# Performance work log

Measured on AMD Instinct MI355X. Metric: run time of the kernel, lower is better.

## Reference

```python
import jax, jax.numpy as jnp
import numpy as np

DIM, NH, WS, SR, CTS = 256, 8, 8, 4, 2
HD = DIM // NH
SCALE = HD ** -0.5

def _linear(x, w, b=None):
    y = x @ w.T
    return y + b if b is not None else y

def _ln(x, g, b, eps=1e-5):
    m = jnp.mean(x, -1, keepdims=True)
    v = jnp.mean((x - m) ** 2, -1, keepdims=True)
    return (x - m) / jnp.sqrt(v + eps) * g + b

def _mlp(x, w1, b1, w2, b2):
    return _linear(jax.nn.gelu(_linear(x, w1, b1), approximate=False), w2, b2)

def _pos_emb_rank3(seq_len, w1, b1, w2):
    # PosEmbMLPSwinv1D with rank=3: coords on cube_root(seq) grid, normalized
    s = int(round(seq_len ** (1.0 / 3.0)))
    c = (jnp.arange(s, dtype=jnp.float32) - s // 2) / (s // 2)
    grid = jnp.stack(jnp.meshgrid(c, c, c, indexing='ij'))      # (3,s,s,s)
    tbl = grid.reshape(3, -1).T                                 # (s^3,3)
    return _linear(jax.nn.relu(_linear(tbl, w1, b1)), w2)[None]  # (1,s^3,dim)

def _rel_bias_3d(ws, w1, b1, w2, n_global):
    # PosEmbMLPSwinv3D: CPB-MLP bias over 3D relative coords, 16*sigmoid, zero-pad for carrier tokens
    r = jnp.arange(-(ws - 1), ws, dtype=jnp.float32)
    tbl = jnp.stack(jnp.meshgrid(r, r, r, indexing='ij'), axis=-1) / (ws - 1)
    tbl = tbl * 8.0
    tbl = jnp.sign(tbl) * jnp.log2(jnp.abs(tbl) + 1.0) / np.log2(8.0)
    table = _linear(jax.nn.relu(_linear(tbl.reshape(-1, 3), w1, b1)), w2)  # ((2ws-1)^3, NH)
    coords = jnp.stack(jnp.meshgrid(jnp.arange(ws), jnp.arange(ws), jnp.arange(ws), indexing='ij'))
    cf = coords.reshape(3, -1)
    rel = (cf[:, :, None] - cf[:, None, :]).transpose(1, 2, 0) + (ws - 1)  # (P,P,3)
    idx = rel[..., 0] * (2 * ws - 1) ** 2 + rel[..., 1] * (2 * ws - 1) + rel[..., 2]
    P = ws ** 3
    bias = table[idx.reshape(-1)].reshape(P, P, NH).transpose(2, 0, 1)
    bias = 16.0 * jax.nn.sigmoid(bias)
    return jnp.pad(bias, ((0, 0), (n_global, 0), (n_global, 0)))[None]  # (1,NH,P+g,P+g)

def _win_attn(x, qkv_w, qkv_b, proj_w, proj_b, bias):
    B, N, C = x.shape
    qkv = _linear(x, qkv_w, qkv_b).reshape(B, N, 3, NH, HD).transpose(2, 0, 3, 1, 4)
    q, k, v = qkv[0], qkv[1], qkv[2]
    attn = jax.nn.softmax(jnp.einsum('bhnd,bhmd->bhnm', q, k) * SCALE + bias, axis=-1)
    out = jnp.einsum('bhnm,bhmd->bhnd', attn, v).transpose(0, 2, 1, 3).reshape(B, N, C)
    return _linear(out, proj_w, proj_b)

def _ct_dewindow(ct, W, H, D, ws):
    bs, _, N = ct.shape
    c = ct.reshape(bs, W // ws, H // ws, D // ws, ws, ws, ws, N)
    c = c.transpose(0, 7, 1, 3, 5, 2, 4, 6).reshape(bs, N, W * H * D)
    return c.transpose(0, 2, 1)

def _ct_window(ct, W, H, D, ws):
    bs, _, N = ct.shape
    c = ct.reshape(bs, H // ws, ws, W // ws, ws, D // ws, ws, N)
    return c.transpose(0, 1, 3, 5, 2, 4, 6, 7)

def setup_inputs() -> dict:
    key = jax.random.key(0)
    ks = jax.random.split(key, 48)
    B0 = 1
    nw = SR ** 3
    def w(k, *s):
        return jax.random.normal(k, s, jnp.float32) * 0.02
    def b(k, *s):
        return jax.random.normal(k, s, jnp.float32) * 0.01
    d4 = 4 * DIM
    return {
        'x': jax.random.normal(ks[0], (B0 * nw, WS ** 3, DIM), jnp.float32),
        'ct': jax.random.normal(ks[1], (B0, (CTS * SR) ** 3, DIM), jnp.float32),
        'pe_w1': w(ks[2], 512, 3), 'pe_b1': b(ks[3], 512), 'pe_w2': w(ks[4], DIM, 512),
        'hpe_w1': w(ks[5], 512, 3), 'hpe_b1': b(ks[6], 512), 'hpe_w2': w(ks[7], DIM, 512),
        'hat_n1_g': jnp.ones((DIM,), jnp.float32), 'hat_n1_b': jnp.zeros((DIM,), jnp.float32),
        'hat_qkv_w': w(ks[8], 3 * DIM, DIM), 'hat_qkv_b': b(ks[9], 3 * DIM),
        'hat_proj_w': w(ks[10], DIM, DIM), 'hat_proj_b': b(ks[11], DIM),
        'hat_cpb_w1': w(ks[12], 512, 3), 'hat_cpb_b1': b(ks[13], 512), 'hat_cpb_w2': w(ks[14], NH, 512),
        'hat_n2_g': jnp.ones((DIM,), jnp.float32), 'hat_n2_b': jnp.zeros((DIM,), jnp.float32),
        'hat_fc1_w': w(ks[15], d4, DIM), 'hat_fc1_b': b(ks[16], d4),
        'hat_fc2_w': w(ks[17], DIM, d4), 'hat_fc2_b': b(ks[18], DIM),
        'n1_g': jnp.ones((DIM,), jnp.float32), 'n1_b': jnp.zeros((DIM,), jnp.float32),
        'qkv_w': w(ks[19], 3 * DIM, DIM), 'qkv_b': b(ks[20], 3 * DIM),
        'proj_w': w(ks[21], DIM, DIM), 'proj_b': b(ks[22], DIM),
        'cpb_w1': w(ks[23], 512, 3), 'cpb_b1': b(ks[24], 512), 'cpb_w2': w(ks[25], NH, 512),
        'n2_g': jnp.ones((DIM,), jnp.float32), 'n2_b': jnp.zeros((DIM,), jnp.float32),
        'fc1_w': w(ks[26], d4, DIM), 'fc1_b': b(ks[27], d4),
        'fc2_w': w(ks[28], DIM, d4), 'fc2_b': b(ks[29], DIM),
    }

def reference(x, ct, pe_w1, pe_b1, pe_w2, hpe_w1, hpe_b1, hpe_w2,
              hat_n1_g, hat_n1_b, hat_qkv_w, hat_qkv_b, hat_proj_w, hat_proj_b,
              hat_cpb_w1, hat_cpb_b1, hat_cpb_w2, hat_n2_g, hat_n2_b,
              hat_fc1_w, hat_fc1_b, hat_fc2_w, hat_fc2_b,
              n1_g, n1_b, qkv_w, qkv_b, proj_w, proj_b,
              cpb_w1, cpb_b1, cpb_w2, n2_g, n2_b, fc1_w, fc1_b, fc2_w, fc2_b):
    Bg, Ng, Hg = ct.shape
    G = CTS * SR  # carrier-token global cube side
    x = x + _pos_emb_rank3(x.shape[1], pe_w1, pe_b1, pe_w2)
    # carrier-token global attention (hierarchical path)
    ct = _ct_dewindow(ct, G, G, G, CTS)
    ct = ct + _pos_emb_rank3(ct.shape[1], hpe_w1, hpe_b1, hpe_w2)
    hat_bias = _rel_bias_3d(G, hat_cpb_w1, hat_cpb_b1, hat_cpb_w2, 0)
    ct = ct + _win_attn(_ln(ct, hat_n1_g, hat_n1_b), hat_qkv_w, hat_qkv_b, hat_proj_w, hat_proj_b, hat_bias)
    ct = ct + _mlp(_ln(ct, hat_n2_g, hat_n2_b), hat_fc1_w, hat_fc1_b, hat_fc2_w, hat_fc2_b)
    ct_w = _ct_window(ct, G, G, G, CTS).reshape(x.shape[0], -1, Hg)
    # windowed attention over [carrier tokens ; window tokens]
    x = jnp.concatenate([ct_w, x], axis=1)
    bias = _rel_bias_3d(WS, cpb_w1, cpb_b1, cpb_w2, CTS ** 3)
    x = x + _win_attn(_ln(x, n1_g, n1_b), qkv_w, qkv_b, proj_w, proj_b, bias)
    x = x + _mlp(_ln(x, n2_g, n2_b), fc1_w, fc1_b, fc2_w, fc2_b)
    split = x.shape[1] - WS ** 3
    ctr, x = x[:, :split], x[:, split:]
    return x, ctr.reshape(Bg, Ng, Hg)
```

## Files before the change

kernel.cpp:

```cpp
#include <hip/hip_runtime.h>
#include <hip/hip_bf16.h>
#include <math.h>

typedef __hip_bfloat16 bf16;

#define SCALE_QK 0.17677669529663687f

__device__ __forceinline__ float b2f(bf16 v){ return __bfloat162float(v); }
__device__ __forceinline__ bf16  f2b(float v){ return __float2bfloat16(v); }
__device__ __forceinline__ short bfs(float x){ bf16 b = f2b(x); short s; __builtin_memcpy(&s, &b, 2); return s; }

struct __align__(16) bf16x8 { bf16 v[8]; };

typedef __attribute__((ext_vector_type(8))) short sh8;
typedef __attribute__((ext_vector_type(4))) short sh4;
typedef __attribute__((ext_vector_type(4))) float f4;

#if defined(__has_builtin)
#if __has_builtin(__builtin_amdgcn_mfma_f32_16x16x16bf16_1k)
#define HAS_MFMA16 1
#else
#define HAS_MFMA16 0
#endif
#else
#define HAS_MFMA16 0
#endif

__global__ __launch_bounds__(256) void wcvt10_k(const float* s0, const float* s1, const float* s2, const float* s3,
                                                const float* s4, const float* s5, const float* s6, const float* s7,
                                                const float* s8, const float* s9,
                                                bf16* d0, bf16* d1, bf16* d2, bf16* d3, bf16* d4,
                                                bf16* d5, bf16* d6, bf16* d7, bf16* d8, bf16* d9) {
    const int sizes[10] = {196608, 65536, 262144, 262144, 196608, 65536, 262144, 262144, 131072, 131072};
    int which = blockIdx.y;
    const float* s; bf16* d;
    switch (which) {
        case 0: s = s0; d = d0; break;  case 1: s = s1; d = d1; break;
        case 2: s = s2; d = d2; break;  case 3: s = s3; d = d3; break;
        case 4: s = s4; d = d4; break;  case 5: s = s5; d = d5; break;
        case 6: s = s6; d = d6; break;  case 7: s = s7; d = d7; break;
        case 8: s = s8; d = d8; break;  default: s = s9; d = d9; break;
    }
    int i = blockIdx.x * 256 + threadIdx.x;
    if (i < sizes[which]) d[i] = f2b(s[i]);
}

__global__ __launch_bounds__(256) void hidbuild_k(const float* __restrict__ w1a, const float* __restrict__ b1a,
                                                  const float* __restrict__ w1b, const float* __restrict__ b1b,
                                                  bf16* __restrict__ hidA, bf16* __restrict__ hidB) {
    const float* w1 = blockIdx.y ? w1b : w1a;
    const float* b1 = blockIdx.y ? b1b : b1a;
    bf16* hid       = blockIdx.y ? hidB : hidA;
    int t = blockIdx.x, tid = threadIdx.x;
    int i = t >> 6, j = (t >> 3) & 7, k = t & 7;
    float c0 = (i - 4) * 0.25f, c1 = (j - 4) * 0.25f, c2 = (k - 4) * 0.25f;
    #pragma unroll
    for (int rep = 0; rep < 2; rep++) {
        int jj = tid + rep * 256;
        float h = c0 * w1[jj*3+0] + c1 * w1[jj*3+1] + c2 * w1[jj*3+2] + b1[jj];
        hid[(size_t)t * 512 + jj] = f2b(fmaxf(h, 0.f));
    }
}

__device__ __forceinline__ float cpb_coord(int idx) {
    float v = (idx - 7) * (8.0f / 7.0f);
    return copysignf(log2f(fabsf(v) + 1.0f) * (1.0f / 3.0f), v);
}
__global__ __launch_bounds__(512) void cpbtab_k(const float* __restrict__ w1a, const float* __restrict__ b1a,
                                                const float* __restrict__ w2a, float* __restrict__ taba,
                                                const float* __restrict__ w1b, const float* __restrict__ b1b,
                                                const float* __restrict__ w2b, float* __restrict__ tabb) {
    const float* w1 = blockIdx.y ? w1b : w1a;
    const float* b1 = blockIdx.y ? b1b : b1a;
    const float* w2 = blockIdx.y ? w2b : w2a;
    float* tab      = blockIdx.y ? tabb : taba;
    int t = blockIdx.x, tid = threadIdx.x;
    __shared__ float hid[512];
    int i = t / 225, r = t - i * 225, j = r / 15, k = r - j * 15;
    float x0 = cpb_coord(i), x1 = cpb_coord(j), x2 = cpb_coord(k);
    float h = x0 * w1[tid*3+0] + x1 * w1[tid*3+1] + x2 * w1[tid*3+2] + b1[tid];
    hid[tid] = fmaxf(h, 0.f);
    __syncthreads();
    int h8 = tid >> 6, lane = tid & 63;
    float p = 0.f;
    for (int jj = lane; jj < 512; jj += 64) p += hid[jj] * w2[h8*512 + jj];
    for (int off = 32; off; off >>= 1) p += __shfl_down(p, off);
    if (lane == 0) tab[t * 8 + h8] = p;
}

__global__ __launch_bounds__(256) void biasbuild_k(const float* __restrict__ taba, float* __restrict__ biasQa,
                                                   const float* __restrict__ tabb, float* __restrict__ biasQb) {
    const float* tab = blockIdx.y ? tabb : taba;
    float* biasQ     = blockIdx.y ? biasQb : biasQa;
    int idx = blockIdx.x * 256 + threadIdx.x;
    int h = idx >> 18, rem = idx & 262143;
    int q = rem >> 9, k = rem & 511;
    int qx = q >> 6, qy = (q >> 3) & 7, qz = q & 7;
    int kx = k >> 6, ky = (k >> 3) & 7, kz = k & 7;
    int tidx = ((qx - kx + 7) * 15 + (qy - ky + 7)) * 15 + (qz - kz + 7);
    float v = tab[tidx * 8 + h];
    biasQ[idx] = 16.f / (1.f + __expf(-v));
}

__global__ __launch_bounds__(256) void ct0build_k(const float* __restrict__ ct_in,
                                                  const float* __restrict__ hpe,
                                                  float* __restrict__ ct0) {
    int u = blockIdx.x, c = threadIdx.x;
    int a = u >> 7, cc = (u >> 5) & 3, e = (u >> 4) & 1, b = (u >> 2) & 3, d = (u >> 1) & 1, f = u & 1;
    int t = a * 128 + b * 32 + cc * 8 + d * 4 + e * 2 + f;
    ct0[(size_t)u * 256 + c] = ct_in[(size_t)t * 256 + c] + hpe[(size_t)u * 256 + c];
}

__global__ __launch_bounds__(256) void ln_k(const float* __restrict__ in,
                                            const float* __restrict__ g,
                                            const float* __restrict__ b,
                                            bf16* __restrict__ out) {
    int row = blockIdx.x, c = threadIdx.x;
    float x = in[(size_t)row * 256 + c];
    float s = x, s2 = x * x;
    for (int off = 32; off; off >>= 1) { s += __shfl_down(s, off); s2 += __shfl_down(s2, off); }
    __shared__ float red[8];
    int wid = c >> 6, lane = c & 63;
    if (lane == 0) { red[wid] = s; red[wid + 4] = s2; }
    __syncthreads();
    if (c == 0) { red[0] = red[0] + red[1] + red[2] + red[3]; red[4] = red[4] + red[5] + red[6] + red[7]; }
    __syncthreads();
    float mean = red[0] * (1.f / 256.f);
    float var  = fmaxf(red[4] * (1.f / 256.f) - mean * mean, 0.f);
    float rstd = rsqrtf(var + 1e-5f);
    out[(size_t)row * 256 + c] = f2b((x - mean) * rstd * g[c] + b[c]);
}

template <int MODE>
__global__ __launch_bounds__(256) void gemm_k(const bf16* __restrict__ A,
                                              const bf16* __restrict__ W,
                                              const float* __restrict__ bias,
                                              int M, int N, int K,
                                              float* __restrict__ res,
                                              bf16* __restrict__ outb) {
    __shared__ short As[128 * 40];
    __shared__ short Ws[128 * 40];
    int m0 = blockIdx.y * 128, n0 = blockIdx.x * 128;
    int tid = threadIdx.x;
    int lane = tid & 63, wave = tid >> 6;
    int quad = lane >> 4, m16 = lane & 15;
    int wm = (wave & 1) * 64, wn = (wave >> 1) * 64;
    int arow = tid >> 2, acol = (tid & 3) * 8;

    f4 acc[4][4];
    #pragma unroll
    for (int i = 0; i < 4; i++)
        #pragma unroll
        for (int j = 0; j < 4; j++) acc[i][j] = (f4){0.f, 0.f, 0.f, 0.f};

    for (int k0 = 0; k0 < K; k0 += 32) {
        sh8 a0 = *reinterpret_cast<const sh8*>(A + (size_t)(m0 + arow) * K + k0 + acol);
        sh8 a1 = *reinterpret_cast<const sh8*>(A + (size_t)(m0 + arow + 64) * K + k0 + acol);
        sh8 w0 = *reinterpret_cast<const sh8*>(W + (size_t)(n0 + arow) * K + k0 + acol);
        sh8 w1 = *reinterpret_cast<const sh8*>(W + (size_t)(n0 + arow + 64) * K + k0 + acol);
        __syncthreads();
        *reinterpret_cast<sh8*>(&As[arow * 40 + acol])        = a0;
        *reinterpret_cast<sh8*>(&As[(arow + 64) * 40 + acol]) = a1;
        *reinterpret_cast<sh8*>(&Ws[arow * 40 + acol])        = w0;
        *reinterpret_cast<sh8*>(&Ws[(arow + 64) * 40 + acol]) = w1;
        __syncthreads();
        sh8 af[4], bf[4];
        #pragma unroll
        for (int mi = 0; mi < 4; mi++)
            af[mi] = *reinterpret_cast<const sh8*>(&As[(wm + mi * 16 + m16) * 40 + quad * 8]);
        #pragma unroll
        for (int ni = 0; ni < 4; ni++)
            bf[ni] = *reinterpret_cast<const sh8*>(&Ws[(wn + ni * 16 + m16) * 40 + quad * 8]);
        #pragma unroll
        for (int mi = 0; mi < 4; mi++)
            #pragma unroll
            for (int ni = 0; ni < 4; ni++)
                acc[mi][ni] = __builtin_amdgcn_mfma_f32_16x16x32_bf16(af[mi], bf[ni], acc[mi][ni], 0, 0, 0);
    }
    (void)M;

    #pragma unroll
    for (int mi = 0; mi < 4; mi++) {
        #pragma unroll
        for (int r = 0; r < 4; r++) {
            int gm = m0 + wm + mi * 16 + quad * 4 + r;
            #pragma unroll
            for (int ni = 0; ni < 4; ni++) {
                int gn = n0 + wn + ni * 16 + m16;
                float v = acc[mi][ni][r];
                if constexpr (MODE != 3) v += bias[gn];
                if constexpr (MODE == 2)      res[(size_t)gm * N + gn] += v;
                else if constexpr (MODE == 3) res[(size_t)gm * N + gn] = v;
                else if constexpr (MODE == 1) outb[(size_t)gm * N + gn] = f2b(0.5f * v * (1.0f + erff(v * 0.70710678118654752f)));
                else                          outb[(size_t)gm * N + gn] = f2b(v);
            }
        }
    }
}

#define VSTR 548
#define FIXM 24.0f
__global__ __launch_bounds__(512) void flash_k(const bf16* __restrict__ qkv,
                                               const float* __restrict__ biasQ,
                                               bf16* __restrict__ out,
                                               int N, int glob) {
    int wh = blockIdx.x, w = wh >> 3, h = wh & 7;
    int qs = blockIdx.y, QS = gridDim.y;
    int tid = threadIdx.x;
    int lane = tid & 63, wave = tid >> 6;
    int quad = lane >> 4, qcol = lane & 15;
    const int NT32 = (N + 31) & ~31;

    __shared__ bf16  Vt[32 * VSTR];
    __shared__ float Osm[8 * 528];
#if !HAS_MFMA16
    __shared__ float Ps[8][16 * 17];
#endif

    for (int i = tid; i < NT32 * 4; i += 512) {
        int tok = i >> 2, seg = i & 3;
        if (tok < N) {
            const bf16* vp = qkv + ((size_t)(w * N + tok)) * 768 + 512 + h * 32 + seg * 8;
            bf16x8 vv = *reinterpret_cast<const bf16x8*>(vp);
            #pragma unroll
            for (int e = 0; e < 8; e++) Vt[(seg * 8 + e) * VSTR + tok] = vv.v[e];
        } else {
            bf16 z = f2b(0.f);
            #pragma unroll
            for (int e = 0; e < 8; e++) Vt[(seg * 8 + e) * VSTR + tok] = z;
        }
    }
    __syncthreads();

    const bf16* qbase = qkv + ((size_t)w * N) * 768 + h * 32;
    const bf16* kbase = qbase + 256;
    int nqt = (N + 15) >> 4, nkt = NT32 >> 5;

    for (int qt = wave + 8 * qs; qt < nqt; qt += 8 * QS) {
        int q_idx = qt * 16 + qcol;
        int q_rd  = (q_idx < N) ? q_idx : (N - 1);
        sh8 qfrag = *reinterpret_cast<const sh8*>(qbase + (size_t)q_rd * 768 + quad * 8);
        f4 O0 = {0.f, 0.f, 0.f, 0.f}, O1 = {0.f, 0.f, 0.f, 0.f};
        float l = 0.f;
        bool qb = (q_idx >= glob) && (q_idx < N);
        const float* brow = biasQ + (((size_t)h << 9) + (size_t)(qb ? (q_idx - glob) : 0)) * 512 - glob;

        for (int kt = 0; kt < nkt; kt++) {
            int bt = kt * 32;
            int k0 = bt + qcol, k1 = bt + 16 + qcol;
            sh8 kf0 = *reinterpret_cast<const sh8*>(kbase + (size_t)((k0 < N) ? k0 : (N - 1)) * 768 + quad * 8);
            sh8 kf1 = *reinterpret_cast<const sh8*>(kbase + (size_t)((k1 < N) ? k1 : (N - 1)) * 768 + quad * 8);
            f4 z = {0.f, 0.f, 0.f, 0.f};
            f4 s0 = __builtin_amdgcn_mfma_f32_16x16x32_bf16(kf0, qfrag, z, 0, 0, 0);
            f4 s1 = __builtin_amdgcn_mfma_f32_16x16x32_bf16(kf1, qfrag, z, 0, 0, 0);

            int tg0 = bt + quad * 4, tg1 = bt + 16 + quad * 4;
            float p[8];
            {
                f4 bb = {0.f, 0.f, 0.f, 0.f};
                if (qb && tg0 >= glob) bb = *reinterpret_cast<const f4*>(brow + tg0);
                bool valid = tg0 < N;
                #pragma unroll
                for (int r = 0; r < 4; r++)
                    p[r] = valid ? __expf(fmaf(s0[r], SCALE_QK, bb[r]) - FIXM) : 0.f;
            }
            {
                f4 bb = {0.f, 0.f, 0.f, 0.f};
                if (qb && tg1 >= glob && tg1 < N) bb = *reinterpret_cast<const f4*>(brow + tg1);
                bool valid = tg1 < N;
                #pragma unroll
                for (int r = 0; r < 4; r++)
                    p[4 + r] = valid ? __expf(fmaf(s1[r], SCALE_QK, bb[r]) - FIXM) : 0.f;
            }
            #pragma unroll
            for (int r = 0; r < 8; r++) l += p[r];

#if HAS_MFMA16
            sh4 pf0, pf1;
            #pragma unroll
            for (int r = 0; r < 4; r++) { pf0[r] = bfs(p[r]); pf1[r] = bfs(p[4 + r]); }
            sh4 v00 = *reinterpret_cast<const sh4*>(&Vt[qcol * VSTR + bt + quad * 4]);
            sh4 v10 = *reinterpret_cast<const sh4*>(&Vt[qcol * VSTR + bt + 16 + quad * 4]);
            sh4 v01 = *reinterpret_cast<const sh4*>(&Vt[(qcol + 16) * VSTR + bt + quad * 4]);
            sh4 v11 = *reinterpret_cast<const sh4*>(&Vt[(qcol + 16) * VSTR + bt + 16 + quad * 4]);
            O0 = __builtin_amdgcn_mfma_f32_16x16x16bf16_1k(v00, pf0, O0, 0, 0, 0);
            O0 = __builtin_amdgcn_mfma_f32_16x16x16bf16_1k(v10, pf1, O0, 0, 0, 0);
            O1 = __builtin_amdgcn_mfma_f32_16x16x16bf16_1k(v01, pf0, O1, 0, 0, 0);
            O1 = __builtin_amdgcn_mfma_f32_16x16x16bf16_1k(v11, pf1, O1, 0, 0, 0);
#else
            for (int half = 0; half < 2; half++) {
                #pragma unroll
                for (int r = 0; r < 4; r++) Ps[wave][(quad * 4 + r) * 17 + qcol] = p[half * 4 + r];
                __builtin_amdgcn_wave_barrier();
                sh8 pbig, va, vb;
                #pragma unroll
                for (int j = 0; j < 8; j++) {
                    int tl = quad * 8 + j;
                    float pv = (quad < 2) ? Ps[wave][tl * 17 + qcol] : 0.f;
                    pbig[j] = bfs(pv);
                    bf16 a0 = (quad < 2) ? Vt[qcol * VSTR + bt + half * 16 + tl] : f2b(0.f);
                    bf16 a1 = (quad < 2) ? Vt[(qcol + 16) * VSTR + bt + half * 16 + tl] : f2b(0.f);
                    short t0, t1;
                    __builtin_memcpy(&t0, &a0, 2); __builtin_memcpy(&t1, &a1, 2);
                    va[j] = t0; vb[j] = t1;
                }
                O0 = __builtin_amdgcn_mfma_f32_16x16x32_bf16(va, pbig, O0, 0, 0, 0);
                O1 = __builtin_amdgcn_mfma_f32_16x16x32_bf16(vb, pbig, O1, 0, 0, 0);
                __builtin_amdgcn_wave_barrier();
            }
#endif
        }

        l += __shfl_xor(l, 16);
        l += __shfl_xor(l, 32);
        float rl = 1.f / l;
        #pragma unroll
        for (int r = 0; r < 4; r++) {
            Osm[wave * 528 + qcol * 33 + quad * 4 + r]      = O0[r] * rl;
            Osm[wave * 528 + qcol * 33 + 16 + quad * 4 + r] = O1[r] * rl;
        }
        __builtin_amdgcn_wave_barrier();
        int row = lane >> 2, dseg = (lane & 3) * 8;
        int q_out = qt * 16 + row;
        if (q_out < N) {
            bf16x8 ov;
            #pragma unroll
            for (int e = 0; e < 8; e++) ov.v[e] = f2b(Osm[wave * 528 + row * 33 + dseg + e]);
            *reinterpret_cast<bf16x8*>(out + ((size_t)(w * N + q_out)) * 256 + h * 32 + dseg) = ov;
        }
        __builtin_amdgcn_wave_barrier();
    }
}

__global__ __launch_bounds__(256) void xcatbuild_k(const float* __restrict__ x_in,
                                                   const float* __restrict__ pe,
                                                   const float* __restrict__ ct2,
                                                   float* __restrict__ xcat) {
    int row = blockIdx.x, w = row / 520, p = row - w * 520, c = threadIdx.x;
    float v;
    if (p < 8) {
        int P = w >> 4, Q = (w >> 2) & 3, R = w & 3;
        int S = p >> 2, T = (p >> 1) & 1, U = p & 1;
        int t = P * 128 + S * 64 + Q * 16 + T * 8 + R * 2 + U;
        v = ct2[(size_t)t * 256 + c];
    } else {
        int t = p - 8;
        v = x_in[((size_t)w * 512 + t) * 256 + c] + pe[(size_t)t * 256 + c];
    }
    xcat[(size_t)row * 256 + c] = v;
}

__global__ __launch_bounds__(256) void outbuild_k(const float* __restrict__ xcat,
                                                  float* __restrict__ out) {
    int row = blockIdx.x, w = row / 520, p = row - w * 520, c = threadIdx.x;
    float v = xcat[(size_t)row * 256 + c];
    if (p >= 8) out[((size_t)(w * 512) + (p - 8)) * 256 + c] = v;
    else        out[(size_t)8388608 + ((size_t)(w * 8) + p) * 256 + c] = v;
}

extern "C" void kernel_launch(void* const* d_in, const int* in_sizes, int n_in,
                              void* d_out, int out_size, void* d_ws, size_t ws_size,
                              hipStream_t stream) {
    const float* x          = (const float*)d_in[0];
    const float* ct         = (const float*)d_in[1];
    const float* pe_w1      = (const float*)d_in[2];
    const float* pe_b1      = (const float*)d_in[3];
    const float* pe_w2      = (const float*)d_in[4];
    const float* hpe_w1     = (const float*)d_in[5];
    const float* hpe_b1     = (const float*)d_in[6];
    const float* hpe_w2     = (const float*)d_in[7];
    const float* hat_n1_g   = (const float*)d_in[8];
    const float* hat_n1_b   = (const float*)d_in[9];
    const float* hat_qkv_w  = (const float*)d_in[10];
    const float* hat_qkv_b  = (const float*)d_in[11];
    const float* hat_proj_w = (const float*)d_in[12];
    const float* hat_proj_b = (const float*)d_in[13];
    const float* hat_cpb_w1 = (const float*)d_in[14];
    const float* hat_cpb_b1 = (const float*)d_in[15];
    const float* hat_cpb_w2 = (const float*)d_in[16];
    const float* hat_n2_g   = (const float*)d_in[17];
    const float* hat_n2_b   = (const float*)d_in[18];
    const float* hat_fc1_w  = (const float*)d_in[19];
    const float* hat_fc1_b  = (const float*)d_in[20];
    const float* hat_fc2_w  = (const float*)d_in[21];
    const float* hat_fc2_b  = (const float*)d_in[22];
    const float* n1_g       = (const float*)d_in[23];
    const float* n1_b       = (const float*)d_in[24];
    const float* qkv_w      = (const float*)d_in[25];
    const float* qkv_b      = (const float*)d_in[26];
    const float* proj_w     = (const float*)d_in[27];
    const float* proj_b     = (const float*)d_in[28];
    const float* cpb_w1     = (const float*)d_in[29];
    const float* cpb_b1     = (const float*)d_in[30];
    const float* cpb_w2     = (const float*)d_in[31];
    const float* n2_g       = (const float*)d_in[32];
    const float* n2_b       = (const float*)d_in[33];
    const float* fc1_w      = (const float*)d_in[34];
    const float* fc1_b      = (const float*)d_in[35];
    const float* fc2_w      = (const float*)d_in[36];
    const float* fc2_b      = (const float*)d_in[37];
    (void)in_sizes; (void)n_in; (void)out_size;

    char* base = (char*)d_ws;
    size_t off = 0;
    auto alloc = [&](size_t bytes) -> void* {
        void* p = base + off;
        off += (bytes + 255) & ~(size_t)255;
        return p;
    };
    float* pe        = (float*)alloc(512 * 256 * 4);
    float* hpe       = (float*)alloc(512 * 256 * 4);
    float* tab_hat   = (float*)alloc(3375 * 8 * 4);
    float* tab2      = (float*)alloc(3375 * 8 * 4);
    float* biasQ2    = (float*)alloc((size_t)8 * 512 * 512 * 4);
    float* ct0       = (float*)alloc(512 * 256 * 4);
    bf16* wb_hqkv  = (bf16*)alloc(768 * 256 * 2);
    bf16* wb_hproj = (bf16*)alloc(256 * 256 * 2);
    bf16* wb_hfc1  = (bf16*)alloc(1024 * 256 * 2);
    bf16* wb_hfc2  = (bf16*)alloc(256 * 1024 * 2);
    bf16* wb_qkv   = (bf16*)alloc(768 * 256 * 2);
    bf16* wb_proj  = (bf16*)alloc(256 * 256 * 2);
    bf16* wb_fc1   = (bf16*)alloc(1024 * 256 * 2);
    bf16* wb_fc2   = (bf16*)alloc(256 * 1024 * 2);
    bf16* wb_pew2  = (bf16*)alloc(256 * 512 * 2);
    bf16* wb_hpew2 = (bf16*)alloc(256 * 512 * 2);
    size_t zstart = off;
    bf16*  hidA      = (bf16*)alloc(512 * 512 * 2);
    bf16*  hidB      = (bf16*)alloc(512 * 512 * 2);
    off = zstart;
    float* biasQ_hat = (float*)alloc((size_t)8 * 512 * 512 * 4);
    bf16*  hct_ln    = (bf16*)alloc(512 * 256 * 2);
    bf16*  hqkv      = (bf16*)alloc(512 * 768 * 2);
    bf16*  hat_attn  = (bf16*)alloc(512 * 256 * 2);
    bf16*  hat_hid   = (bf16*)alloc(512 * 1024 * 2);
    off = zstart;
    float* xcat      = (float*)alloc((size_t)64 * 520 * 256 * 4);
    const int S     = (ws_size >= (size_t)150 * 1024 * 1024) ? 1 : 4;
    const int rows  = 33280 / S;
    const int wins  = 64 / S;
    bf16*  xln_b     = (bf16*)alloc((size_t)rows * 256 * 2);
    char*  region_qa = (char*)alloc((size_t)rows * 1024 * 2);
    bf16*  qkv_b_    = (bf16*)region_qa;
    bf16*  attn_b    = (bf16*)(region_qa + (size_t)rows * 768 * 2);
    bf16*  hidden    = (bf16*)region_qa;

    wcvt10_k<<<dim3(1024, 10), 256, 0, stream>>>(hat_qkv_w, hat_proj_w, hat_fc1_w, hat_fc2_w,
                                                 qkv_w, proj_w, fc1_w, fc2_w, pe_w2, hpe_w2,
                                                 wb_hqkv, wb_hproj, wb_hfc1, wb_hfc2,
                                                 wb_qkv, wb_proj, wb_fc1, wb_fc2, wb_pew2, wb_hpew2);

    hidbuild_k<<<dim3(512, 2), 256, 0, stream>>>(pe_w1, pe_b1, hpe_w1, hpe_b1, hidA, hidB);
    gemm_k<3><<<dim3(2, 4), 256, 0, stream>>>(hidA, wb_pew2,  nullptr, 512, 256, 512, pe,  nullptr);
    gemm_k<3><<<dim3(2, 4), 256, 0, stream>>>(hidB, wb_hpew2, nullptr, 512, 256, 512, hpe, nullptr);

    cpbtab_k<<<dim3(3375, 2), 512, 0, stream>>>(hat_cpb_w1, hat_cpb_b1, hat_cpb_w2, tab_hat,
                                                cpb_w1, cpb_b1, cpb_w2, tab2);
    biasbuild_k<<<dim3(8192, 2), 256, 0, stream>>>(tab_hat, biasQ_hat, tab2, biasQ2);

    ct0build_k<<<512, 256, 0, stream>>>(ct, hpe, ct0);
    ln_k<<<512, 256, 0, stream>>>(ct0, hat_n1_g, hat_n1_b, hct_ln);
    gemm_k<0><<<dim3(6, 4), 256, 0, stream>>>(hct_ln, wb_hqkv, hat_qkv_b, 512, 768, 256, nullptr, hqkv);
    flash_k<<<dim3(8, 4), 512, 0, stream>>>(hqkv, biasQ_hat, hat_attn, 512, 0);
    gemm_k<2><<<dim3(2, 4), 256, 0, stream>>>(hat_attn, wb_hproj, hat_proj_b, 512, 256, 256, ct0, nullptr);
    ln_k<<<512, 256, 0, stream>>>(ct0, hat_n2_g, hat_n2_b, hct_ln);
    gemm_k<1><<<dim3(8, 4), 256, 0, stream>>>(hct_ln, wb_hfc1, hat_fc1_b, 512, 1024, 256, nullptr, hat_hid);
    gemm_k<2><<<dim3(2, 4), 256, 0, stream>>>(hat_hid, wb_hfc2, hat_fc2_b, 512, 256, 1024, ct0, nullptr);

    xcatbuild_k<<<33280, 256, 0, stream>>>(x, pe, ct0, xcat);

    for (int s = 0; s < S; s++) {
        float* xc = xcat + (size_t)s * rows * 256;
        ln_k<<<rows, 256, 0, stream>>>(xc, n1_g, n1_b, xln_b);
        gemm_k<0><<<dim3(6, rows / 128), 256, 0, stream>>>(xln_b, wb_qkv, qkv_b, rows, 768, 256, nullptr, qkv_b_);
        flash_k<<<dim3(wins * 8, 5), 512, 0, stream>>>(qkv_b_, biasQ2, attn_b, 520, 8);
        gemm_k<2><<<dim3(2, rows / 128), 256, 0, stream>>>(attn_b, wb_proj, proj_b, rows, 256, 256, xc, nullptr);
    }
    for (int s = 0; s < S; s++) {
        float* xc = xcat + (size_t)s * rows * 256;
        ln_k<<<rows, 256, 0, stream>>>(xc, n2_g, n2_b, xln_b);
        gemm_k<1><<<dim3(8, rows / 128), 256, 0, stream>>>(xln_b, wb_fc1, fc1_b, rows, 1024, 256, nullptr, hidden);
        gemm_k<2><<<dim3(2, rows / 128), 256, 0, stream>>>(hidden, wb_fc2, fc2_b, rows, 256, 1024, xc, nullptr);
    }

    outbuild_k<<<33280, 256, 0, stream>>>(xcat, (float*)d_out);
}
```

Baseline: 648.0 us.

## Process two query tiles per wave in flash attention and prefetch K fragments

```diff
diff --git a/kernel.cpp b/kernel.cpp
--- a/kernel.cpp
+++ b/kernel.cpp
@@ -235,98 +235,154 @@
     const bf16* qbase = qkv + ((size_t)w * N) * 768 + h * 32;
     const bf16* kbase = qbase + 256;
     int nqt = (N + 15) >> 4, nkt = NT32 >> 5;
-
-    for (int qt = wave + 8 * qs; qt < nqt; qt += 8 * QS) {
-        int q_idx = qt * 16 + qcol;
-        int q_rd  = (q_idx < N) ? q_idx : (N - 1);
-        sh8 qfrag = *reinterpret_cast<const sh8*>(qbase + (size_t)q_rd * 768 + quad * 8);
-        f4 O0 = {0.f, 0.f, 0.f, 0.f}, O1 = {0.f, 0.f, 0.f, 0.f};
-        float l = 0.f;
-        bool qb = (q_idx >= glob) && (q_idx < N);
-        const float* brow = biasQ + (((size_t)h << 9) + (size_t)(qb ? (q_idx - glob) : 0)) * 512 - glob;
+    int npt = (nqt + 1) >> 1;
+
+    for (int pp = wave + 8 * qs; pp < npt; pp += 8 * QS) {
+        int qA = pp * 32 + qcol;
+        int qB = qA + 16;
+        int qrA = (qA < N) ? qA : (N - 1);
+        int qrB = (qB < N) ? qB : (N - 1);
+        sh8 qfA = *reinterpret_cast<const sh8*>(qbase + (size_t)qrA * 768 + quad * 8);
+        sh8 qfB = *reinterpret_cast<const sh8*>(qbase + (size_t)qrB * 768 + quad * 8);
+        f4 O0A = {0.f,0.f,0.f,0.f}, O1A = {0.f,0.f,0.f,0.f};
+        f4 O0B = {0.f,0.f,0.f,0.f}, O1B = {0.f,0.f,0.f,0.f};
+        float lA = 0.f, lB = 0.f;
+        bool vA = (qA >= glob) && (qA < N);
+        bool vB = (qB >= glob) && (qB < N);
+        const float* browA = biasQ + (((size_t)h << 9) + (size_t)(vA ? (qA - glob) : 0)) * 512 - glob;
+        const float* browB = biasQ + (((size_t)h << 9) + (size_t)(vB ? (qB - glob) : 0)) * 512 - glob;
+
+        sh8 kf0, kf1;
+        {
+            int k0 = qcol, k1 = 16 + qcol;
+            kf0 = *reinterpret_cast<const sh8*>(kbase + (size_t)((k0 < N) ? k0 : (N - 1)) * 768 + quad * 8);
+            kf1 = *reinterpret_cast<const sh8*>(kbase + (size_t)((k1 < N) ? k1 : (N - 1)) * 768 + quad * 8);
+        }
 
         for (int kt = 0; kt < nkt; kt++) {
             int bt = kt * 32;
-            int k0 = bt + qcol, k1 = bt + 16 + qcol;
-            sh8 kf0 = *reinterpret_cast<const sh8*>(kbase + (size_t)((k0 < N) ? k0 : (N - 1)) * 768 + quad * 8);
-            sh8 kf1 = *reinterpret_cast<const sh8*>(kbase + (size_t)((k1 < N) ? k1 : (N - 1)) * 768 + quad * 8);
+            sh8 c0 = kf0, c1 = kf1;
+            if (kt + 1 < nkt) {
+                int n0 = bt + 32 + qcol, n1 = bt + 48 + qcol;
+                kf0 = *reinterpret_cast<const sh8*>(kbase + (size_t)((n0 < N) ? n0 : (N - 1)) * 768 + quad * 8);
+                kf1 = *reinterpret_cast<const sh8*>(kbase + (size_t)((n1 < N) ? n1 : (N - 1)) * 768 + quad * 8);
+            }
             f4 z = {0.f, 0.f, 0.f, 0.f};
-            f4 s0 = __builtin_amdgcn_mfma_f32_16x16x32_bf16(kf0, qfrag, z, 0, 0, 0);
-            f4 s1 = __builtin_amdgcn_mfma_f32_16x16x32_bf16(kf1, qfrag, z, 0, 0, 0);
+            f4 s0A = __builtin_amdgcn_mfma_f32_16x16x32_bf16(c0, qfA, z, 0, 0, 0);
+            f4 s1A = __builtin_amdgcn_mfma_f32_16x16x32_bf16(c1, qfA, z, 0, 0, 0);
+            f4 s0B = __builtin_amdgcn_mfma_f32_16x16x32_bf16(c0, qfB, z, 0, 0, 0);
+            f4 s1B = __builtin_amdgcn_mfma_f32_16x16x32_bf16(c1, qfB, z, 0, 0, 0);
 
             int tg0 = bt + quad * 4, tg1 = bt + 16 + quad * 4;
-            float p[8];
-            {
-                f4 bb = {0.f, 0.f, 0.f, 0.f};
-                if (qb && tg0 >= glob) bb = *reinterpret_cast<const f4*>(brow + tg0);
-                bool valid = tg0 < N;
-                #pragma unroll
-                for (int r = 0; r < 4; r++)
-                    p[r] = valid ? __expf(fmaf(s0[r], SCALE_QK, bb[r]) - FIXM) : 0.f;
-            }
-            {
-                f4 bb = {0.f, 0.f, 0.f, 0.f};
-                if (qb && tg1 >= glob && tg1 < N) bb = *reinterpret_cast<const f4*>(brow + tg1);
-                bool valid = tg1 < N;
-                #pragma unroll
-                for (int r = 0; r < 4; r++)
-                    p[4 + r] = valid ? __expf(fmaf(s1[r], SCALE_QK, bb[r]) - FIXM) : 0.f;
-            }
-            #pragma unroll
-            for (int r = 0; r < 8; r++) l += p[r];
+            bool val0 = tg0 < N, val1 = tg1 < N;
+            f4 bb0A = z, bb1A = z, bb0B = z, bb1B = z;
+            if (vA && tg0 >= glob)               bb0A = *reinterpret_cast<const f4*>(browA + tg0);
+            if (vA && tg1 >= glob && tg1 < N)    bb1A = *reinterpret_cast<const f4*>(browA + tg1);
+            if (vB && tg0 >= glob)               bb0B = *reinterpret_cast<const f4*>(browB + tg0);
+            if (vB && tg1 >= glob && tg1 < N)    bb1B = *reinterpret_cast<const f4*>(browB + tg1);
+
+            float pA0[4], pA1[4], pB0[4], pB1[4];
+            #pragma unroll
+            for (int r = 0; r < 4; r++) {
+                pA0[r] = val0 ? __expf(fmaf(s0A[r], SCALE_QK, bb0A[r]) - FIXM) : 0.f;
+                pA1[r] = val1 ? __expf(fmaf(s1A[r], SCALE_QK, bb1A[r]) - FIXM) : 0.f;
+                pB0[r] = val0 ? __expf(fmaf(s0B[r], SCALE_QK, bb0B[r]) - FIXM) : 0.f;
+                pB1[r] = val1 ? __expf(fmaf(s1B[r], SCALE_QK, bb1B[r]) - FIXM) : 0.f;
+            }
+            #pragma unroll
+            for (int r = 0; r < 4; r++) { lA += pA0[r] + pA1[r]; lB += pB0[r] + pB1[r]; }
 
 #if HAS_MFMA16
-            sh4 pf0, pf1;
-            #pragma unroll
-            for (int r = 0; r < 4; r++) { pf0[r] = bfs(p[r]); pf1[r] = bfs(p[4 + r]); }
+            sh4 pf0A, pf1A, pf0B, pf1B;
+            #pragma unroll
+            for (int r = 0; r < 4; r++) {
+                pf0A[r] = bfs(pA0[r]); pf1A[r] = bfs(pA1[r]);
+                pf0B[r] = bfs(pB0[r]); pf1B[r] = bfs(pB1[r]);
+            }
             sh4 v00 = *reinterpret_cast<const sh4*>(&Vt[qcol * VSTR + bt + quad * 4]);
             sh4 v10 = *reinterpret_cast<const sh4*>(&Vt[qcol * VSTR + bt + 16 + quad * 4]);
             sh4 v01 = *reinterpret_cast<const sh4*>(&Vt[(qcol + 16) * VSTR + bt + quad * 4]);
             sh4 v11 = *reinterpret_cast<const sh4*>(&Vt[(qcol + 16) * VSTR + bt + 16 + quad * 4]);
-            O0 = __builtin_amdgcn_mfma_f32_16x16x16bf16_1k(v00, pf0, O0, 0, 0, 0);
-            O0 = __builtin_amdgcn_mfma_f32_16x16x16bf16_1k(v10, pf1, O0, 0, 0, 0);
-            O1 = __builtin_amdgcn_mfma_f32_16x16x16bf16_1k(v01, pf0, O1, 0, 0, 0);
-            O1 = __builtin_amdgcn_mfma_f32_16x16x16bf16_1k(v11, pf1, O1, 0, 0, 0);
+            O0A = __builtin_amdgcn_mfma_f32_16x16x16bf16_1k(v00, pf0A, O0A, 0, 0, 0);
+            O0A = __builtin_amdgcn_mfma_f32_16x16x16bf16_1k(v10, pf1A, O0A, 0, 0, 0);
+            O1A = __builtin_amdgcn_mfma_f32_16x16x16bf16_1k(v01, pf0A, O1A, 0, 0, 0);
+            O1A = __builtin_amdgcn_mfma_f32_16x16x16bf16_1k(v11, pf1A, O1A, 0, 0, 0);
+            O0B = __builtin_amdgcn_mfma_f32_16x16x16bf16_1k(v00, pf0B, O0B, 0, 0, 0);
+            O0B = __builtin_amdgcn_mfma_f32_16x16x16bf16_1k(v10, pf1B, O0B, 0, 0, 0);
+            O1B = __builtin_amdgcn_mfma_f32_16x16x16bf16_1k(v01, pf0B, O1B, 0, 0, 0);
+            O1B = __builtin_amdgcn_mfma_f32_16x16x16bf16_1k(v11, pf1B, O1B, 0, 0, 0);
 #else
-            for (int half = 0; half < 2; half++) {
+            {
+                const float* phA[2] = {pA0, pA1};
+                const float* phB[2] = {pB0, pB1};
+                for (int t = 0; t < 2; t++) {
+                    const float* const* ph = t ? phB : phA;
+                    for (int half = 0; half < 2; half++) {
+                        #pragma unroll
+                        for (int r = 0; r < 4; r++) Ps[wave][(quad * 4 + r) * 17 + qcol] = ph[half][r];
+                        __builtin_amdgcn_wave_barrier();
+                        sh8 pbig, va, vb;
+                        #pragma unroll
+                        for (int j = 0; j < 8; j++) {
+                            int tl = quad * 8 + j;
+                            float pv = (quad < 2) ? Ps[wave][tl * 17 + qcol] : 0.f;
+                            pbig[j] = bfs(pv);
+                            bf16 a0 = (quad < 2) ? Vt[qcol * VSTR + bt + half * 16 + tl] : f2b(0.f);
+                            bf16 a1 = (quad < 2) ? Vt[(qcol + 16) * VSTR + bt + half * 16 + tl] : f2b(0.f);
+                            short t0, t1;
+                            __builtin_memcpy(&t0, &a0, 2); __builtin_memcpy(&t1, &a1, 2);
+                            va[j] = t0; vb[j] = t1;
+                        }
+                        if (t == 0) {
+                            O0A = __builtin_amdgcn_mfma_f32_16x16x32_bf16(va, pbig, O0A, 0, 0, 0);
+                            O1A = __builtin_amdgcn_mfma_f32_16x16x32_bf16(vb, pbig, O1A, 0, 0, 0);
+                        } else {
+                            O0B = __builtin_amdgcn_mfma_f32_16x16x32_bf16(va, pbig, O0B, 0, 0, 0);
+                            O1B = __builtin_amdgcn_mfma_f32_16x16x32_bf16(vb, pbig, O1B, 0, 0, 0);
+                        }
+                        __builtin_amdgcn_wave_barrier();
+                    }
+                }
+            }
+#endif
+        }
+
+        lA += __shfl_xor(lA, 16); lA += __shfl_xor(lA, 32);
+        lB += __shfl_xor(lB, 16); lB += __shfl_xor(lB, 32);
+        float rlA = 1.f / lA, rlB = 1.f / lB;
+        int row = lane >> 2, dseg = (lane & 3) * 8;
+
+        #pragma unroll
+        for (int r = 0; r < 4; r++) {
+            Osm[wave * 528 + qcol * 33 + quad * 4 + r]      = O0A[r] * rlA;
+            Osm[wave * 528 + qcol * 33 + 16 + quad * 4 + r] = O1A[r] * rlA;
+        }
+        __builtin_amdgcn_wave_barrier();
+        {
+            int q_out = pp * 32 + row;
+            if (q_out < N) {
+                bf16x8 ov;
                 #pragma unroll
-                for (int r = 0; r < 4; r++) Ps[wave][(quad * 4 + r) * 17 + qcol] = p[half * 4 + r];
-                __builtin_amdgcn_wave_barrier();
-                sh8 pbig, va, vb;
+                for (int e = 0; e < 8; e++) ov.v[e] = f2b(Osm[wave * 528 + row * 33 + dseg + e]);
+                *reinterpret_cast<bf16x8*>(out + ((size_t)(w * N + q_out)) * 256 + h * 32 + dseg) = ov;
+            }
+        }
+        __builtin_amdgcn_wave_barrier();
+
+        #pragma unroll
+        for (int r = 0; r < 4; r++) {
+            Osm[wave * 528 + qcol * 33 + quad * 4 + r]      = O0B[r] * rlB;
+            Osm[wave * 528 + qcol * 33 + 16 + quad * 4 + r] = O1B[r] * rlB;
+        }
+        __builtin_amdgcn_wave_barrier();
+        {
+            int q_out = pp * 32 + 16 + row;
+            if (q_out < N) {
+                bf16x8 ov;
                 #pragma unroll
-                for (int j = 0; j < 8; j++) {
-                    int tl = quad * 8 + j;
-                    float pv = (quad < 2) ? Ps[wave][tl * 17 + qcol] : 0.f;
-                    pbig[j] = bfs(pv);
-                    bf16 a0 = (quad < 2) ? Vt[qcol * VSTR + bt + half * 16 + tl] : f2b(0.f);
-                    bf16 a1 = (quad < 2) ? Vt[(qcol + 16) * VSTR + bt + half * 16 + tl] : f2b(0.f);
-                    short t0, t1;
-                    __builtin_memcpy(&t0, &a0, 2); __builtin_memcpy(&t1, &a1, 2);
-                    va[j] = t0; vb[j] = t1;
-                }
-                O0 = __builtin_amdgcn_mfma_f32_16x16x32_bf16(va, pbig, O0, 0, 0, 0);
-                O1 = __builtin_amdgcn_mfma_f32_16x16x32_bf16(vb, pbig, O1, 0, 0, 0);
-                __builtin_amdgcn_wave_barrier();
-            }
-#endif
-        }
-
-        l += __shfl_xor(l, 16);
-        l += __shfl_xor(l, 32);
-        float rl = 1.f / l;
-        #pragma unroll
-        for (int r = 0; r < 4; r++) {
-            Osm[wave * 528 + qcol * 33 + quad * 4 + r]      = O0[r] * rl;
-            Osm[wave * 528 + qcol * 33 + 16 + quad * 4 + r] = O1[r] * rl;
-        }
-        __builtin_amdgcn_wave_barrier();
-        int row = lane >> 2, dseg = (lane & 3) * 8;
-        int q_out = qt * 16 + row;
-        if (q_out < N) {
-            bf16x8 ov;
-            #pragma unroll
-            for (int e = 0; e < 8; e++) ov.v[e] = f2b(Osm[wave * 528 + row * 33 + dseg + e]);
-            *reinterpret_cast<bf16x8*>(out + ((size_t)(w * N + q_out)) * 256 + h * 32 + dseg) = ov;
+                for (int e = 0; e < 8; e++) ov.v[e] = f2b(Osm[wave * 528 + row * 33 + dseg + e]);
+                *reinterpret_cast<bf16x8*>(out + ((size_t)(w * N + q_out)) * 256 + h * 32 + dseg) = ov;
+            }
         }
         __builtin_amdgcn_wave_barrier();
     }
@@ -460,7 +516,7 @@
     ct0build_k<<<512, 256, 0, stream>>>(ct, hpe, ct0);
     ln_k<<<512, 256, 0, stream>>>(ct0, hat_n1_g, hat_n1_b, hct_ln);
     gemm_k<0><<<dim3(6, 4), 256, 0, stream>>>(hct_ln, wb_hqkv, hat_qkv_b, 512, 768, 256, nullptr, hqkv);
-    flash_k<<<dim3(8, 4), 512, 0, stream>>>(hqkv, biasQ_hat, hat_attn, 512, 0);
+    flash_k<<<dim3(8, 2), 512, 0, stream>>>(hqkv, biasQ_hat, hat_attn, 512, 0);
     gemm_k<2><<<dim3(2, 4), 256, 0, stream>>>(hat_attn, wb_hproj, hat_proj_b, 512, 256, 256, ct0, nullptr);
     ln_k<<<512, 256, 0, stream>>>(ct0, hat_n2_g, hat_n2_b, hct_ln);
     gemm_k<1><<<dim3(8, 4), 256, 0, stream>>>(hct_ln, wb_hfc1, hat_fc1_b, 512, 1024, 256, nullptr, hat_hid);
@@ -472,7 +528,7 @@
         float* xc = xcat + (size_t)s * rows * 256;
         ln_k<<<rows, 256, 0, stream>>>(xc, n1_g, n1_b, xln_b);
         gemm_k<0><<<dim3(6, rows / 128), 256, 0, stream>>>(xln_b, wb_qkv, qkv_b, rows, 768, 256, nullptr, qkv_b_);
-        flash_k<<<dim3(wins * 8, 5), 512, 0, stream>>>(qkv_b_, biasQ2, attn_b, 520, 8);
+        flash_k<<<dim3(wins * 8, 2), 512, 0, stream>>>(qkv_b_, biasQ2, attn_b, 520, 8);
         gemm_k<2><<<dim3(2, rows / 128), 256, 0, stream>>>(attn_b, wb_proj, proj_b, rows, 256, 256, xc, nullptr);
     }
     for (int s = 0; s < S; s++) {
```

Measured after the change: 621.0 us. -4.2%, faster.
